# Performance work log

Measured on AMD Instinct MI355X. Metric: run time of the kernel, lower is better.

Reference implementation:

```python
import jax, jax.numpy as jnp
import numpy as np

N = 4194304  # batch size
EPS = 1e-5   # BatchNorm1d default eps


def setup_inputs() -> dict:
    key = jax.random.key(0)
    ks = jax.random.split(key, 16)
    s = 0.3  # small init scale for weights
    return {
        "x": jax.random.normal(ks[0], (N, 5), dtype=jnp.float32),
        # 8 stacked 5x5 linear layers (PyTorch convention: W is [out, in])
        "lins_w": jax.random.normal(ks[1], (8, 5, 5), dtype=jnp.float32) * s,
        "lins_b": jax.random.normal(ks[2], (8, 5), dtype=jnp.float32) * s,
        # 4 stacked 5x5 skip linear layers
        "skips_w": jax.random.normal(ks[3], (4, 5, 5), dtype=jnp.float32) * s,
        "skips_b": jax.random.normal(ks[4], (4, 5), dtype=jnp.float32) * s,
        # 8 BatchNorm1d(5) affine params
        "bn_g": jnp.ones((8, 5), dtype=jnp.float32),
        "bn_b": jnp.zeros((8, 5), dtype=jnp.float32),
        # lin9: 5->2, bn9: BatchNorm1d(2), lin10: 2->1
        "lin9_w": jax.random.normal(ks[5], (2, 5), dtype=jnp.float32) * s,
        "lin9_b": jax.random.normal(ks[6], (2,), dtype=jnp.float32) * s,
        "bn9_g": jnp.ones((2,), dtype=jnp.float32),
        "bn9_b": jnp.zeros((2,), dtype=jnp.float32),
        "lin10_w": jax.random.normal(ks[7], (1, 2), dtype=jnp.float32) * s,
        "lin10_b": jax.random.normal(ks[8], (1,), dtype=jnp.float32) * s,
    }


def _lin(x, w, b):
    # PyTorch Linear: y = x @ W^T + b
    return x @ w.T + b


def _bn(x, g, b):
    # BatchNorm1d in training mode: biased batch stats over the batch dim
    mu = jnp.mean(x, axis=0)
    var = jnp.mean(jnp.square(x - mu), axis=0)
    return (x - mu) * jax.lax.rsqrt(var + EPS) * g + b


def reference(x, lins_w, lins_b, skips_w, skips_b, bn_g, bn_b,
              lin9_w, lin9_b, bn9_g, bn9_b, lin10_w, lin10_b):
    relu = jax.nn.relu
    z = x
    # 4 residual blocks, each consuming two Linear+BN layers and one skip Linear
    for blk in range(4):
        i, j = 2 * blk, 2 * blk + 1
        skip = _lin(z, skips_w[blk], skips_b[blk])
        h = relu(_bn(_lin(z, lins_w[i], lins_b[i]), bn_g[i], bn_b[i]))
        z = relu(_bn(_lin(h, lins_w[j], lins_b[j]), bn_g[j], bn_b[j]) + skip)
    z9 = relu(_bn(_lin(z, lin9_w, lin9_b), bn9_g, bn9_b))
    out = _lin(z9, lin10_w, lin10_b)  # [N, 1]
    return out
```

## Files before the change

kernel.cpp:

```cpp
#include <hip/hip_runtime.h>
#include <hip/hip_fp16.h>
#include <math.h>

#define NROWS 4194304
#define M4Q   (NROWS/4)
#define EPSV  1e-5f

#define BLK   512
#define THR   256
#define TOT   (BLK*THR)
#define GPT   (M4Q/TOT)

#define SLOTS 32
#define SSTR  (SLOTS*32)
#define STATS_BYTES (9*SSTR*4)
#define ZBYTES_H ((size_t)5*M4Q*8)


struct __align__(8) h4 { __half2 lo, hi; };

__device__ __forceinline__ h4 f4_to_h4(const float4& f){
  h4 r; r.lo = __floats2half2_rn(f.x, f.y); r.hi = __floats2half2_rn(f.z, f.w);
  return r;
}
__device__ __forceinline__ float4 h4_to_f4(const h4& h){
  float2 a = __half22float2(h.lo), b = __half22float2(h.hi);
  return make_float4(a.x, a.y, b.x, b.y);
}

__device__ __forceinline__ float4 mk4(float v){ return make_float4(v,v,v,v); }
__device__ __forceinline__ float4 fma44(float a, const float4& b, const float4& c){
  return make_float4(fmaf(a,b.x,c.x), fmaf(a,b.y,c.y), fmaf(a,b.z,c.z), fmaf(a,b.w,c.w));
}
__device__ __forceinline__ float4 relu4(const float4& a){
  return make_float4(fmaxf(a.x,0.f),fmaxf(a.y,0.f),fmaxf(a.z,0.f),fmaxf(a.w,0.f));
}

__device__ __forceinline__ void acc_stats(const float4 z[5], float acc[20]){
  #pragma unroll
  for(int d=0; d<5; ++d) acc[d] += (z[d].x + z[d].y) + (z[d].z + z[d].w);
  int k = 5;
  #pragma unroll
  for(int d=0; d<5; ++d){
    #pragma unroll
    for(int e=d; e<5; ++e){
      acc[k] += z[d].x*z[e].x + z[d].y*z[e].y + z[d].z*z[e].z + z[d].w*z[e].w;
      ++k;
    }
  }
}

__device__ __forceinline__ void fold_generic(const float* __restrict__ sums,
                                             const float* __restrict__ W,
                                             const float* __restrict__ g,
                                             const float* __restrict__ be,
                                             int c, float invN,
                                             float* Arow, float* cout){
  float mu[5];
  #pragma unroll
  for(int d=0;d<5;++d) mu[d] = sums[d]*invN;
  float wr[5];
  #pragma unroll
  for(int d=0;d<5;++d) wr[d] = W[c*5+d];
  float m = 0.f, v = 0.f;
  #pragma unroll
  for(int d=0;d<5;++d){
    m += wr[d]*mu[d];
    #pragma unroll
    for(int e=0;e<5;++e){
      const int dd = d<e?d:e, ee = d<e?e:d;
      const float cov = sums[5 + dd*5+ee - (dd*(dd+1))/2]*invN - mu[d]*mu[e];
      v += wr[d]*wr[e]*cov;
    }
  }
  const float s = g[c] / sqrtf(v + EPSV);
  #pragma unroll
  for(int d=0;d<5;++d) Arow[d] = s*wr[d];
  *cout = be[c] - s*m;
}

__device__ __forceinline__ void reduce_slots(float acc[20], float* stage){
  #pragma unroll
  for(int k=0;k<20;++k){
    float v = acc[k];
    #pragma unroll
    for(int m=32;m>=1;m>>=1) v += __shfl_xor(v, m);
    acc[k] = v;
  }
  __shared__ float red[(THR/64)*20];
  const int lane = threadIdx.x & 63, wv = threadIdx.x >> 6;
  if(lane==0){
    #pragma unroll
    for(int k=0;k<20;++k) red[wv*20+k] = acc[k];
  }
  __syncthreads();
  if(threadIdx.x < 20){
    float s = 0.f;
    #pragma unroll
    for(int w=0; w<THR/64; ++w) s += red[w*20 + threadIdx.x];
    atomicAdd(stage + (blockIdx.x & (SLOTS-1))*32 + threadIdx.x, s);
  }
}

__device__ __forceinline__ void sum_slots(const float* __restrict__ stage, float* raw){
  if(threadIdx.x < 20){
    float s = 0.f;
    #pragma unroll
    for(int j=0;j<SLOTS;++j) s += stage[j*32 + (int)threadIdx.x];
    raw[threadIdx.x] = s;
  }
  __syncthreads();
}

__global__ __launch_bounds__(THR)
void k_init(const float* __restrict__ x, h4* __restrict__ zbuf,
            float* __restrict__ stats){
  const int tid = blockIdx.x*THR + threadIdx.x;
  float acc[20];
  #pragma unroll
  for(int k=0;k<20;++k) acc[k]=0.f;
  #pragma unroll 2
  for(int g=0; g<GPT; ++g){
    const int G = tid + g*TOT;
    union { float4 v[5]; float f[20]; } u;
    const float4* xp = (const float4*)x + (size_t)G*5;
    #pragma unroll
    for(int q=0;q<5;++q) u.v[q] = xp[q];
    float4 z[5];
    #pragma unroll
    for(int c=0;c<5;++c) z[c] = make_float4(u.f[c], u.f[5+c], u.f[10+c], u.f[15+c]);
    #pragma unroll
    for(int c=0;c<5;++c){
      h4 hz = f4_to_h4(z[c]);
      zbuf[c*M4Q + G] = hz;
      z[c] = h4_to_f4(hz);
    }
    acc_stats(z, acc);
  }
  reduce_slots(acc, stats + 0*SSTR);
}

__global__ __launch_bounds__(THR)
void k_statsH(const h4* __restrict__ zbuf, float* __restrict__ stats,
              const float* __restrict__ lins_w, const float* __restrict__ bn_g,
              const float* __restrict__ bn_b, int b){
  const int i = 2*b, j = i+1;
  __shared__ float raw[20];
  __shared__ float F1s[30];
  sum_slots(stats + i*SSTR, raw);
  if(threadIdx.x < 5)
    fold_generic(raw, lins_w+25*i, bn_g+5*i, bn_b+5*i, (int)threadIdx.x,
                 1.0f/(float)NROWS, &F1s[threadIdx.x*5], &F1s[25+threadIdx.x]);
  __syncthreads();
  float f1[30];
  #pragma unroll
  for(int k=0;k<30;++k) f1[k] = F1s[k];
  const int tid = blockIdx.x*THR + threadIdx.x;
  float acc[20];
  #pragma unroll
  for(int k=0;k<20;++k) acc[k]=0.f;
  #pragma unroll 2
  for(int g=0; g<GPT; ++g){
    const int G = tid + g*TOT;
    float4 z[5], h[5];
    #pragma unroll
    for(int c=0;c<5;++c) z[c] = h4_to_f4(zbuf[c*M4Q + G]);
    #pragma unroll
    for(int c=0;c<5;++c){
      float4 u = mk4(f1[25+c]);
      #pragma unroll
      for(int d=0;d<5;++d) u = fma44(f1[c*5+d], z[d], u);
      h[c] = relu4(u);
    }
    acc_stats(h, acc);
  }
  reduce_slots(acc, stats + j*SSTR);
}

__global__ __launch_bounds__(THR)
void k_updateZ(h4* __restrict__ zbuf, float* __restrict__ stats,
               const float* __restrict__ lins_w, const float* __restrict__ bn_g,
               const float* __restrict__ bn_b, const float* __restrict__ skips_w,
               const float* __restrict__ skips_b, int b){
  const int i = 2*b, j = i+1;
  __shared__ float rawA[20], rawB[20];
  __shared__ float F1s[30], F2s[30], SWs[25];
  sum_slots(stats + i*SSTR, rawA);
  sum_slots(stats + j*SSTR, rawB);
  if(threadIdx.x < 5){
    fold_generic(rawA, lins_w+25*i, bn_g+5*i, bn_b+5*i, (int)threadIdx.x,
                 1.0f/(float)NROWS, &F1s[threadIdx.x*5], &F1s[25+threadIdx.x]);
    fold_generic(rawB, lins_w+25*j, bn_g+5*j, bn_b+5*j, (int)threadIdx.x,
                 1.0f/(float)NROWS, &F2s[threadIdx.x*5], &F2s[25+threadIdx.x]);
    F2s[25+threadIdx.x] += skips_b[5*b + threadIdx.x];
  }
  if(threadIdx.x >= 64 && threadIdx.x < 89)
    SWs[threadIdx.x-64] = skips_w[25*b + (threadIdx.x-64)];
  __syncthreads();
  float f1[30], f2[30], sw[25];
  #pragma unroll
  for(int k=0;k<30;++k){ f1[k]=F1s[k]; f2[k]=F2s[k]; }
  #pragma unroll
  for(int k=0;k<25;++k) sw[k]=SWs[k];
  const int tid = blockIdx.x*THR + threadIdx.x;
  float acc[20];
  #pragma unroll
  for(int k=0;k<20;++k) acc[k]=0.f;
  #pragma unroll 2
  for(int g=0; g<GPT; ++g){
    const int G = tid + g*TOT;
    float4 z[5], h[5], t[5];
    #pragma unroll
    for(int c=0;c<5;++c) z[c] = h4_to_f4(zbuf[c*M4Q + G]);
    #pragma unroll
    for(int c=0;c<5;++c){
      float4 u = mk4(f1[25+c]);
      #pragma unroll
      for(int d=0;d<5;++d) u = fma44(f1[c*5+d], z[d], u);
      h[c] = relu4(u);
    }
    #pragma unroll
    for(int c=0;c<5;++c){
      float4 u = mk4(f2[25+c]);
      #pragma unroll
      for(int d=0;d<5;++d){
        u = fma44(f2[c*5+d], h[d], u);
        u = fma44(sw[c*5+d], z[d], u);
      }
      t[c] = relu4(u);
    }
    #pragma unroll
    for(int c=0;c<5;++c){
      h4 hz = f4_to_h4(t[c]);
      zbuf[c*M4Q + G] = hz;
      t[c] = h4_to_f4(hz);
    }
    acc_stats(t, acc);
  }
  reduce_slots(acc, stats + (i+2)*SSTR);
}

__global__ __launch_bounds__(THR)
void k_final(const h4* __restrict__ zbuf, const float* __restrict__ stats,
             const float* __restrict__ lin9_w, const float* __restrict__ bn9_g,
             const float* __restrict__ bn9_b, const float* __restrict__ lin10_w,
             const float* __restrict__ lin10_b, float* __restrict__ out){
  __shared__ float raw[20];
  __shared__ float A9c[12];
  sum_slots(stats + 8*SSTR, raw);
  if(threadIdx.x < 2)
    fold_generic(raw, lin9_w, bn9_g, bn9_b, (int)threadIdx.x,
                 1.0f/(float)NROWS, &A9c[threadIdx.x*5], &A9c[10+threadIdx.x]);
  __syncthreads();
  float f9[12];
  #pragma unroll
  for(int k=0;k<12;++k) f9[k] = A9c[k];
  const float w10a = lin10_w[0], w10b = lin10_w[1], b10 = lin10_b[0];
  const int tid = blockIdx.x*THR + threadIdx.x;
  #pragma unroll 2
  for(int g=0; g<GPT; ++g){
    const int G = tid + g*TOT;
    float4 z[5];
    #pragma unroll
    for(int c=0;c<5;++c) z[c] = h4_to_f4(zbuf[c*M4Q + G]);
    float4 u0 = mk4(f9[10]), u1 = mk4(f9[11]);
    #pragma unroll
    for(int d=0;d<5;++d){ u0 = fma44(f9[d], z[d], u0); u1 = fma44(f9[5+d], z[d], u1); }
    u0 = relu4(u0); u1 = relu4(u1);
    float4 o = mk4(b10);
    o = fma44(w10a, u0, o);
    o = fma44(w10b, u1, o);
    ((float4*)out)[G] = o;
  }
}

__global__ __launch_bounds__(THR)
void k_fromx(const float* __restrict__ x, float* __restrict__ stats,
             const float* __restrict__ lins_w, const float* __restrict__ bn_g,
             const float* __restrict__ bn_b, const float* __restrict__ skips_w,
             const float* __restrict__ skips_b, const float* __restrict__ lin9_w,
             const float* __restrict__ bn9_g, const float* __restrict__ bn9_b,
             const float* __restrict__ lin10_w, const float* __restrict__ lin10_b,
             float* __restrict__ out, int target, int do_final){
  __shared__ float rawAll[9][20];
  __shared__ float FA[8][30];
  __shared__ float SW[100];
  __shared__ float A9c[12];
  const int tix = threadIdx.x;
  const int nf = do_final ? 9 : target;
  if(tix < 20*nf){
    const int L = tix/20, k = tix%20;
    float s = 0.f;
    #pragma unroll
    for(int j=0;j<SLOTS;++j) s += stats[L*SSTR + j*32 + k];
    rawAll[L][k] = s;
  }
  __syncthreads();
  const int nlay = do_final ? 8 : (target < 8 ? target : 8);
  if(tix < 5*nlay){
    const int L = tix/5, c = tix%5;
    fold_generic(&rawAll[L][0], lins_w+25*L, bn_g+5*L, bn_b+5*L, c,
                 1.0f/(float)NROWS, &FA[L][c*5], &FA[L][25+c]);
    if(L & 1) FA[L][25+c] += skips_b[(L>>1)*5 + c];
  } else if(tix >= 64 && tix < 164){
    SW[tix-64] = skips_w[tix-64];
  }
  if(do_final && tix >= 40 && tix < 42){
    const int c = tix-40;
    fold_generic(&rawAll[8][0], lin9_w, bn9_g, bn9_b, c,
                 1.0f/(float)NROWS, &A9c[c*5], &A9c[10+c]);
  }
  __syncthreads();
  float w10a=0.f, w10b=0.f, b10=0.f;
  if(do_final){ w10a = lin10_w[0]; w10b = lin10_w[1]; b10 = lin10_b[0]; }
  float acc[20];
  #pragma unroll
  for(int k=0;k<20;++k) acc[k]=0.f;
  const int gid = blockIdx.x*THR + tix;
  const int steps = do_final ? 8 : target;
  for(int t0=gid; t0<M4Q; t0+=TOT){
    union { float4 v[5]; float f[20]; } u;
    const float4* xp = (const float4*)x + (size_t)t0*5;
    #pragma unroll
    for(int q=0;q<5;++q) u.v[q] = xp[q];
    float4 z[5], h[5];
    #pragma unroll
    for(int c=0;c<5;++c) z[c] = make_float4(u.f[c], u.f[5+c], u.f[10+c], u.f[15+c]);
    #pragma unroll 1
    for(int s=1; s<=steps; ++s){
      const int L = s-1, b = L>>1;
      if(s & 1){
        #pragma unroll
        for(int c=0;c<5;++c){
          float4 t2 = mk4(FA[L][25+c]);
          #pragma unroll
          for(int d=0;d<5;++d) t2 = fma44(FA[L][c*5+d], z[d], t2);
          h[c] = relu4(t2);
        }
      } else {
        float4 zn[5];
        #pragma unroll
        for(int c=0;c<5;++c){
          float4 t2 = mk4(FA[L][25+c]);
          #pragma unroll
          for(int d=0;d<5;++d){
            t2 = fma44(FA[L][c*5+d], h[d], t2);
            t2 = fma44(SW[b*25+c*5+d], z[d], t2);
          }
          zn[c] = relu4(t2);
        }
        #pragma unroll
        for(int c=0;c<5;++c) z[c] = zn[c];
      }
    }
    if(do_final){
      float4 u0 = mk4(A9c[10]), u1 = mk4(A9c[11]);
      #pragma unroll
      for(int d=0;d<5;++d){ u0 = fma44(A9c[d], z[d], u0); u1 = fma44(A9c[5+d], z[d], u1); }
      u0 = relu4(u0); u1 = relu4(u1);
      float4 o = mk4(b10);
      o = fma44(w10a, u0, o);
      o = fma44(w10b, u1, o);
      ((float4*)out)[t0] = o;
    } else {
      if(steps & 1) acc_stats(h, acc);
      else          acc_stats(z, acc);
    }
  }
  if(!do_final) reduce_slots(acc, stats + target*SSTR);
}

extern "C" void kernel_launch(void* const* d_in, const int* in_sizes, int n_in,
                              void* d_out, int out_size, void* d_ws, size_t ws_size,
                              hipStream_t stream){
  (void)in_sizes; (void)n_in; (void)out_size;
  const float* x       = (const float*)d_in[0];
  const float* lins_w  = (const float*)d_in[1];
  const float* skips_w = (const float*)d_in[3];
  const float* skips_b = (const float*)d_in[4];
  const float* bn_g    = (const float*)d_in[5];
  const float* bn_b    = (const float*)d_in[6];
  const float* lin9_w  = (const float*)d_in[7];
  const float* bn9_g   = (const float*)d_in[9];
  const float* bn9_b   = (const float*)d_in[10];
  const float* lin10_w = (const float*)d_in[11];
  const float* lin10_b = (const float*)d_in[12];
  float* out = (float*)d_out;

  if(ws_size >= ZBYTES_H + (size_t)STATS_BYTES){
    h4*    zbuf  = (h4*)d_ws;
    float* stats = (float*)((char*)d_ws + ZBYTES_H);
    hipMemsetAsync(stats, 0, STATS_BYTES, stream);
    k_init<<<BLK, THR, 0, stream>>>(x, zbuf, stats);
    for(int b=0;b<4;++b){
      k_statsH <<<BLK, THR, 0, stream>>>(zbuf, stats, lins_w, bn_g, bn_b, b);
      k_updateZ<<<BLK, THR, 0, stream>>>(zbuf, stats, lins_w, bn_g, bn_b,
                                         skips_w, skips_b, b);
    }
    k_final<<<BLK, THR, 0, stream>>>(zbuf, stats, lin9_w, bn9_g, bn9_b,
                                     lin10_w, lin10_b, out);
  } else {
    float* stats = (float*)d_ws;
    hipMemsetAsync(stats, 0, STATS_BYTES, stream);
    for(int s=0; s<=8; ++s)
      k_fromx<<<BLK, THR, 0, stream>>>(x, stats, lins_w, bn_g, bn_b, skips_w,
                                       skips_b, lin9_w, bn9_g, bn9_b, lin10_w,
                                       lin10_b, out, s, 0);
    k_fromx<<<BLK, THR, 0, stream>>>(x, stats, lins_w, bn_g, bn_b, skips_w,
                                     skips_b, lin9_w, bn9_g, bn9_b, lin10_w,
                                     lin10_b, out, 8, 1);
  }
}
```

Before: 318.3 us.

## Pack fp16 activations into 16-byte planes, double grid, force uniform coefficients

Changes the fp16 activation buffer from five separate 8-byte planes to two 16-byte interleaved planes plus one 8-byte plane. Each thread then issues three wider loads and stores instead of five. The grid and stats slot count are doubled to raise occupancy and spread atomic contention. Broadcast coefficients are wrapped in readfirstlane so they live in scalar registers, which frees vector registers. The trade-off is more blocks and more slot-reduction work per kernel.

```diff
diff --git a/kernel.cpp b/kernel.cpp
--- a/kernel.cpp
+++ b/kernel.cpp
@@ -6,18 +6,23 @@
 #define M4Q   (NROWS/4)
 #define EPSV  1e-5f
 
-#define BLK   512
+#define BLK   1024
 #define THR   256
 #define TOT   (BLK*THR)
 #define GPT   (M4Q/TOT)
 
-#define SLOTS 32
+#define SLOTS 64
 #define SSTR  (SLOTS*32)
 #define STATS_BYTES (9*SSTR*4)
-#define ZBYTES_H ((size_t)5*M4Q*8)
-
-
-struct __align__(8) h4 { __half2 lo, hi; };
+
+#define ZAB_OFF 0
+#define ZCD_OFF ((size_t)M4Q*16)
+#define ZE_OFF  ((size_t)M4Q*32)
+#define ZBYTES_H ((size_t)M4Q*40)
+
+
+struct __align__(8)  h4   { __half2 lo, hi; };
+struct __align__(16) h4x2 { h4 a, b; };
 
 __device__ __forceinline__ h4 f4_to_h4(const float4& f){
   h4 r; r.lo = __floats2half2_rn(f.x, f.y); r.hi = __floats2half2_rn(f.z, f.w);
@@ -34,6 +39,29 @@
 }
 __device__ __forceinline__ float4 relu4(const float4& a){
   return make_float4(fmaxf(a.x,0.f),fmaxf(a.y,0.f),fmaxf(a.z,0.f),fmaxf(a.w,0.f));
+}
+__device__ __forceinline__ float uni(float v){
+  return __uint_as_float((unsigned)__builtin_amdgcn_readfirstlane((int)__float_as_uint(v)));
+}
+
+__device__ __forceinline__ void z_load(const char* ws, int G, float4 z[5]){
+  const h4x2 p01 = ((const h4x2*)(ws + ZAB_OFF))[G];
+  const h4x2 p23 = ((const h4x2*)(ws + ZCD_OFF))[G];
+  const h4   p4  = ((const h4*)  (ws + ZE_OFF ))[G];
+  z[0]=h4_to_f4(p01.a); z[1]=h4_to_f4(p01.b);
+  z[2]=h4_to_f4(p23.a); z[3]=h4_to_f4(p23.b);
+  z[4]=h4_to_f4(p4);
+}
+__device__ __forceinline__ void z_store(char* ws, int G, float4 z[5]){
+  h4x2 p01; p01.a=f4_to_h4(z[0]); p01.b=f4_to_h4(z[1]);
+  h4x2 p23; p23.a=f4_to_h4(z[2]); p23.b=f4_to_h4(z[3]);
+  h4   p4 = f4_to_h4(z[4]);
+  ((h4x2*)(ws + ZAB_OFF))[G]=p01;
+  ((h4x2*)(ws + ZCD_OFF))[G]=p23;
+  ((h4*)  (ws + ZE_OFF ))[G]=p4;
+  z[0]=h4_to_f4(p01.a); z[1]=h4_to_f4(p01.b);
+  z[2]=h4_to_f4(p23.a); z[3]=h4_to_f4(p23.b);
+  z[4]=h4_to_f4(p4);
 }
 
 __device__ __forceinline__ void acc_stats(const float4 z[5], float acc[20]){
@@ -105,7 +133,7 @@
 __device__ __forceinline__ void sum_slots(const float* __restrict__ stage, float* raw){
   if(threadIdx.x < 20){
     float s = 0.f;
-    #pragma unroll
+    #pragma unroll 8
     for(int j=0;j<SLOTS;++j) s += stage[j*32 + (int)threadIdx.x];
     raw[threadIdx.x] = s;
   }
@@ -113,7 +141,7 @@
 }
 
 __global__ __launch_bounds__(THR)
-void k_init(const float* __restrict__ x, h4* __restrict__ zbuf,
+void k_init(const float* __restrict__ x, char* __restrict__ zws,
             float* __restrict__ stats){
   const int tid = blockIdx.x*THR + threadIdx.x;
   float acc[20];
@@ -129,19 +157,14 @@
     float4 z[5];
     #pragma unroll
     for(int c=0;c<5;++c) z[c] = make_float4(u.f[c], u.f[5+c], u.f[10+c], u.f[15+c]);
-    #pragma unroll
-    for(int c=0;c<5;++c){
-      h4 hz = f4_to_h4(z[c]);
-      zbuf[c*M4Q + G] = hz;
-      z[c] = h4_to_f4(hz);
-    }
+    z_store(zws, G, z);
     acc_stats(z, acc);
   }
   reduce_slots(acc, stats + 0*SSTR);
 }
 
 __global__ __launch_bounds__(THR)
-void k_statsH(const h4* __restrict__ zbuf, float* __restrict__ stats,
+void k_statsH(const char* __restrict__ zws, float* __restrict__ stats,
               const float* __restrict__ lins_w, const float* __restrict__ bn_g,
               const float* __restrict__ bn_b, int b){
   const int i = 2*b, j = i+1;
@@ -154,7 +177,7 @@
   __syncthreads();
   float f1[30];
   #pragma unroll
-  for(int k=0;k<30;++k) f1[k] = F1s[k];
+  for(int k=0;k<30;++k) f1[k] = uni(F1s[k]);
   const int tid = blockIdx.x*THR + threadIdx.x;
   float acc[20];
   #pragma unroll
@@ -163,8 +186,7 @@
   for(int g=0; g<GPT; ++g){
     const int G = tid + g*TOT;
     float4 z[5], h[5];
-    #pragma unroll
-    for(int c=0;c<5;++c) z[c] = h4_to_f4(zbuf[c*M4Q + G]);
+    z_load(zws, G, z);
     #pragma unroll
     for(int c=0;c<5;++c){
       float4 u = mk4(f1[25+c]);
@@ -178,7 +200,7 @@
 }
 
 __global__ __launch_bounds__(THR)
-void k_updateZ(h4* __restrict__ zbuf, float* __restrict__ stats,
+void k_updateZ(char* __restrict__ zws, float* __restrict__ stats,
                const float* __restrict__ lins_w, const float* __restrict__ bn_g,
                const float* __restrict__ bn_b, const float* __restrict__ skips_w,
                const float* __restrict__ skips_b, int b){
@@ -199,9 +221,9 @@
   __syncthreads();
   float f1[30], f2[30], sw[25];
   #pragma unroll
-  for(int k=0;k<30;++k){ f1[k]=F1s[k]; f2[k]=F2s[k]; }
-  #pragma unroll
-  for(int k=0;k<25;++k) sw[k]=SWs[k];
+  for(int k=0;k<30;++k){ f1[k]=uni(F1s[k]); f2[k]=uni(F2s[k]); }
+  #pragma unroll
+  for(int k=0;k<25;++k) sw[k]=uni(SWs[k]);
   const int tid = blockIdx.x*THR + threadIdx.x;
   float acc[20];
   #pragma unroll
@@ -210,8 +232,7 @@
   for(int g=0; g<GPT; ++g){
     const int G = tid + g*TOT;
     float4 z[5], h[5], t[5];
-    #pragma unroll
-    for(int c=0;c<5;++c) z[c] = h4_to_f4(zbuf[c*M4Q + G]);
+    z_load(zws, G, z);
     #pragma unroll
     for(int c=0;c<5;++c){
       float4 u = mk4(f1[25+c]);
@@ -229,19 +250,14 @@
       }
       t[c] = relu4(u);
     }
-    #pragma unroll
-    for(int c=0;c<5;++c){
-      h4 hz = f4_to_h4(t[c]);
-      zbuf[c*M4Q + G] = hz;
-      t[c] = h4_to_f4(hz);
-    }
+    z_store(zws, G, t);
     acc_stats(t, acc);
   }
   reduce_slots(acc, stats + (i+2)*SSTR);
 }
 
 __global__ __launch_bounds__(THR)
-void k_final(const h4* __restrict__ zbuf, const float* __restrict__ stats,
+void k_final(const char* __restrict__ zws, const float* __restrict__ stats,
              const float* __restrict__ lin9_w, const float* __restrict__ bn9_g,
              const float* __restrict__ bn9_b, const float* __restrict__ lin10_w,
              const float* __restrict__ lin10_b, float* __restrict__ out){
@@ -254,15 +270,14 @@
   __syncthreads();
   float f9[12];
   #pragma unroll
-  for(int k=0;k<12;++k) f9[k] = A9c[k];
-  const float w10a = lin10_w[0], w10b = lin10_w[1], b10 = lin10_b[0];
+  for(int k=0;k<12;++k) f9[k] = uni(A9c[k]);
+  const float w10a = uni(lin10_w[0]), w10b = uni(lin10_w[1]), b10 = uni(lin10_b[0]);
   const int tid = blockIdx.x*THR + threadIdx.x;
   #pragma unroll 2
   for(int g=0; g<GPT; ++g){
     const int G = tid + g*TOT;
     float4 z[5];
-    #pragma unroll
-    for(int c=0;c<5;++c) z[c] = h4_to_f4(zbuf[c*M4Q + G]);
+    z_load(zws, G, z);
     float4 u0 = mk4(f9[10]), u1 = mk4(f9[11]);
     #pragma unroll
     for(int d=0;d<5;++d){ u0 = fma44(f9[d], z[d], u0); u1 = fma44(f9[5+d], z[d], u1); }
@@ -291,7 +306,7 @@
   if(tix < 20*nf){
     const int L = tix/20, k = tix%20;
     float s = 0.f;
-    #pragma unroll
+    #pragma unroll 8
     for(int j=0;j<SLOTS;++j) s += stats[L*SSTR + j*32 + k];
     rawAll[L][k] = s;
   }
@@ -388,16 +403,16 @@
   float* out = (float*)d_out;
 
   if(ws_size >= ZBYTES_H + (size_t)STATS_BYTES){
-    h4*    zbuf  = (h4*)d_ws;
+    char*  zws   = (char*)d_ws;
     float* stats = (float*)((char*)d_ws + ZBYTES_H);
     hipMemsetAsync(stats, 0, STATS_BYTES, stream);
-    k_init<<<BLK, THR, 0, stream>>>(x, zbuf, stats);
+    k_init<<<BLK, THR, 0, stream>>>(x, zws, stats);
     for(int b=0;b<4;++b){
-      k_statsH <<<BLK, THR, 0, stream>>>(zbuf, stats, lins_w, bn_g, bn_b, b);
-      k_updateZ<<<BLK, THR, 0, stream>>>(zbuf, stats, lins_w, bn_g, bn_b,
+      k_statsH <<<BLK, THR, 0, stream>>>(zws, stats, lins_w, bn_g, bn_b, b);
+      k_updateZ<<<BLK, THR, 0, stream>>>(zws, stats, lins_w, bn_g, bn_b,
                                          skips_w, skips_b, b);
     }
-    k_final<<<BLK, THR, 0, stream>>>(zbuf, stats, lin9_w, bn9_g, bn9_b,
+    k_final<<<BLK, THR, 0, stream>>>(zws, stats, lin9_w, bn9_g, bn9_b,
                                      lin10_w, lin10_b, out);
   } else {
     float* stats = (float*)d_ws;
```

Measured after the change: 333.3 us. 4.7% more time.
